# Kernel optimization log

Measured on AMD Instinct MI355X. Metric: run time of the kernel, lower is better.

## Reference

```python
import jax, jax.numpy as jnp
import numpy as np

STRIDES = (2, 2, 2)  # from init strides
BN_EPS = 1e-3        # keras BatchNormalization default epsilon


def upsample3d(x, s):
    # x: [B, D, H, W, C] -> nearest-neighbor repeat, like keras UpSampling3D
    x = jnp.repeat(x, s[0], axis=1)
    x = jnp.repeat(x, s[1], axis=2)
    return jnp.repeat(x, s[2], axis=3)


def _conv3d_same(xi, wi):
    # xi: [D, H, W, C]; wi: [kd, kh, kw, Cin, Cout] -> SAME, stride 1
    return jax.lax.conv_general_dilated(
        xi[None], wi, window_strides=(1, 1, 1), padding='SAME',
        dimension_numbers=('NDHWC', 'DHWIO', 'NDHWC'))[0]


# per-sample dynamic conv: each batch element uses its own hypernet kernel
per_sample_conv3d = jax.vmap(_conv3d_same, in_axes=(0, 0))


def batchnorm_train(x, gamma, beta):
    # training-mode BN over N,D,H,W axes
    mean = jnp.mean(x, axis=(0, 1, 2, 3), keepdims=True)
    var = jnp.var(x, axis=(0, 1, 2, 3), keepdims=True)
    return gamma * (x - mean) * jax.lax.rsqrt(var + BN_EPS) + beta


def setup_inputs() -> dict:
    key = jax.random.key(0)
    k1, k2, k3, k4 = jax.random.split(key, 4)
    B, D, H, W, Cin, Cmid = 4, 8, 32, 32, 128, 64
    x = jax.random.normal(k1, (B, D, H, W, Cin), dtype=jnp.float32)
    # scale kernels like fan-in init to keep activations sane
    w1 = jax.random.normal(k2, (B, 3, 3, 3, Cin, Cmid), dtype=jnp.float32) * 0.02
    w2 = jax.random.normal(k3, (B, 3, 3, 3, 2 * Cmid, Cmid), dtype=jnp.float32) * 0.02
    skip = jax.random.normal(k4, (B, 2 * D, 2 * H, 2 * W, Cmid), dtype=jnp.float32)
    return {
        'x': x, 'w1': w1, 'w2': w2, 'skip': skip,
        'gamma1': jnp.ones((Cmid,), jnp.float32),
        'beta1': jnp.zeros((Cmid,), jnp.float32),
        'gamma2': jnp.ones((Cmid,), jnp.float32),
        'beta2': jnp.zeros((Cmid,), jnp.float32),
        'training': 1,
    }


def reference(x, w1, w2, skip, gamma1, beta1, gamma2, beta2, training):
    x = upsample3d(x, STRIDES)                       # [B, 2D, 2H, 2W, Cin]
    x = per_sample_conv3d(x, w1)                     # [B, 2D, 2H, 2W, Cmid]
    x = batchnorm_train(x, gamma1, beta1)
    x = jax.nn.relu(x)
    x = jnp.concatenate([x, skip], axis=-1)          # [B, 2D, 2H, 2W, 2*Cmid]
    x = per_sample_conv3d(x, w2)                     # [B, 2D, 2H, 2W, Cmid]
    x = batchnorm_train(x, gamma2, beta2)
    return jax.nn.relu(x)
```

## Files before the change

kernel.cpp:

```cpp
#include <hip/hip_runtime.h>


typedef __attribute__((ext_vector_type(8))) short short8;
typedef __attribute__((ext_vector_type(4))) float f32x4;

__device__ __forceinline__ float bf2f(unsigned short u) {
  union { unsigned int i; float f; } v; v.i = ((unsigned int)u) << 16; return v.f;
}
__device__ __forceinline__ unsigned short f2b(float f) {
  union { float ff; unsigned int u; } v; v.ff = f;
  unsigned int x = v.u;
  return (unsigned short)((x + 0x7FFFu + ((x >> 16) & 1u)) >> 16);
}
__device__ __forceinline__ unsigned int pk2(float a, float b) {
  return (unsigned int)f2b(a) | ((unsigned int)f2b(b) << 16);
}
__device__ __forceinline__ void gload16(const void* g, void* l) {
  __builtin_amdgcn_global_load_lds(
      (const __attribute__((address_space(1))) void*)g,
      (__attribute__((address_space(3))) void*)l, 16, 0, 0);
}

#define ASTR 136
#define WSTR 132

__global__ __launch_bounds__(256) void hg_prep_k(
    const float* __restrict__ x, const float* __restrict__ skip,
    const float* __restrict__ w1, const float* __restrict__ w2,
    unsigned short* __restrict__ xb, unsigned short* __restrict__ skb,
    unsigned short* __restrict__ wt2, unsigned short* __restrict__ wc1,
    float* __restrict__ sums) {
  __shared__ short T[64 * ASTR];
  int blk = blockIdx.x;
  int tid = threadIdx.x;
  if (blk < 10240) {
    const float* s; unsigned short* d; size_t i;
    if (blk < 8192) { s = skip; d = skb; i = ((size_t)blk * 256 + tid) << 3; }
    else            { s = x;    d = xb;  i = ((size_t)(blk - 8192) * 256 + tid) << 3; }
    float4 a = *(const float4*)(s + i);
    float4 c = *(const float4*)(s + i + 4);
    uint4 o;
    o.x = pk2(a.x, a.y); o.y = pk2(a.z, a.w);
    o.z = pk2(c.x, c.y); o.w = pk2(c.z, c.w);
    *(uint4*)(d + i) = o;
  } else if (blk < 10348) {
    int bt = blk - 10240;
    const float* src = w2 + (size_t)bt * 8192;
    int co = tid & 63, c0 = tid >> 6;
    for (int i = 0; i < 32; ++i) {
      int ci = c0 + (i << 2);
      T[co * ASTR + ci] = (short)f2b(src[(size_t)ci * 64 + co]);
    }
    __syncthreads();
    unsigned short* dst = wt2 + (size_t)bt * 8192;
    for (int i = 0; i < 4; ++i) {
      int task = tid + (i << 8);
      int row = task >> 4, q = task & 15;
      *(uint4*)(dst + row * 128 + (q << 3)) = *(const uint4*)&T[row * ASTR + (q << 3)];
    }
  } else if (blk < 10604) {
    int m9 = blk - 10348;
    int b = m9 >> 6, m = m9 & 63;
    int dd = m >> 4, hh = (m >> 2) & 3, ww = m & 3;
    const int ks[4] = {0, 1, 0, 2}, kc[4] = {1, 2, 2, 1};
    int co = tid & 63, c0 = tid >> 6;
    const float* wb = w1 + (size_t)b * 27 * 8192;
    for (int i = 0; i < 32; ++i) {
      int ci = c0 + (i << 2);
      float s = 0.f;
      for (int a = 0; a < kc[dd]; ++a)
        for (int e = 0; e < kc[hh]; ++e)
          for (int c = 0; c < kc[ww]; ++c) {
            int tap = ((ks[dd] + a) * 3 + ks[hh] + e) * 3 + ks[ww] + c;
            s += wb[(size_t)tap * 8192 + (size_t)ci * 64 + co];
          }
      T[co * ASTR + ci] = (short)f2b(s);
    }
    __syncthreads();
    unsigned short* dst = wc1 + (size_t)m9 * 8192;
    for (int i = 0; i < 4; ++i) {
      int task = tid + (i << 8);
      int row = task >> 4, q = task & 15;
      *(uint4*)(dst + row * 128 + (q << 3)) = *(const uint4*)&T[row * ASTR + (q << 3)];
    }
  } else {
    for (int i = tid; i < 2112; i += 256) sums[i] = 0.f;
  }
}

__global__ __launch_bounds__(256, 3) void hg_c1p_k(
    const unsigned short* __restrict__ xb, const unsigned short* __restrict__ wc1,
    const unsigned short* __restrict__ zb, unsigned short* __restrict__ outb,
    float* __restrict__ sums) {
  __shared__ short Xl[2 * 100 * 128];
  int tid = threadIdx.x;
  int xcd = blockIdx.x & 7, slot = blockIdx.x >> 3;
  int b = xcd & 3;
  int t = ((xcd >> 2) << 7) + slot;
  int od = t >> 4, hti = (t >> 2) & 3, wti = t & 3;
  int pd = od & 1, md = od >> 1;
  int lane = tid & 63, quad = lane >> 4, l16 = lane & 15;
  int wid = tid >> 6;
  int ph = wid >> 1, pw = wid & 1;

  for (int pl = 0; pl < 2; ++pl) {
    int sd = md + pd - 1 + pl;
    int dok = ((unsigned)sd < 8u);
    for (int i = 0; i < 7; ++i) {
      int task = tid + (i << 8);
      if (task < 1600) {
        int pos = task >> 4, pq = task & 15;
        int q = (pq & 8) | ((pq & 7) ^ (pos & 7));
        int sh = pos / 10, sw = pos - sh * 10;
        int h = (hti << 3) + sh - 1, w = (wti << 3) + sw - 1;
        const unsigned short* src = zb;
        if (dok && (unsigned)h < 32u && (unsigned)w < 32u)
          src = xb + ((((size_t)(b * 8 + sd)) * 32 + h) * 32 + w) * 128 + (q << 3);
        gload16(src, (char*)Xl + ((pl * 1600 + (i << 8) + (tid & 192)) << 4));
      }
    }
  }
  __syncthreads();

  f32x4 acc[4][4];
#pragma unroll
  for (int i = 0; i < 4; ++i)
#pragma unroll
    for (int j = 0; j < 4; ++j) acc[i][j] = (f32x4){0.f, 0.f, 0.f, 0.f};

  const unsigned short* wcb = wc1 + ((size_t)b * 64 + (pd << 5) + (ph << 3) + (pw << 1)) * 8192;

  for (int td = 0; td < 2; ++td) {
    const char* Xp = (const char*)Xl + td * 25600;
    for (int th = 0; th < 2; ++th) {
      int hb = ph + th;
      for (int tw = 0; tw < 2; ++tw) {
        int wb2 = pw + tw;
        const unsigned short* wp = wcb + (size_t)((td << 4) + (th << 2) + tw) * 8192;
#pragma unroll
        for (int ksx = 0; ksx < 4; ++ksx) {
          int cq = (ksx << 2) + quad;
          short8 av[4], bv[4];
#pragma unroll
          for (int mt = 0; mt < 4; ++mt) {
            int pos = ((mt << 1) + (l16 >> 3) + hb) * 10 + (l16 & 7) + wb2;
            int pc = (cq & 8) | ((cq & 7) ^ (pos & 7));
            av[mt] = *(const short8*)(Xp + pos * 256 + (pc << 4));
          }
#pragma unroll
          for (int nt = 0; nt < 4; ++nt)
            bv[nt] = *(const short8*)(wp + ((nt << 4) + l16) * 128 + (cq << 3));
#pragma unroll
          for (int mt = 0; mt < 4; ++mt)
#pragma unroll
            for (int nt = 0; nt < 4; ++nt)
              acc[mt][nt] = __builtin_amdgcn_mfma_f32_16x16x32_bf16(
                  av[mt], bv[nt], acc[mt][nt], 0, 0, 0);
        }
      }
    }
  }

  __syncthreads();
  float* sbf = (float*)Xl;
  int rowb = (b * 16 + od) * 64;
#pragma unroll
  for (int nt = 0; nt < 4; ++nt) {
    int n = (nt << 4) + l16;
    float s = 0.f, q2 = 0.f;
#pragma unroll
    for (int mt = 0; mt < 4; ++mt) {
      int mh = (mt << 1) + (quad >> 1);
      int oh = (((hti << 3) + mh) << 1) + ph;
      size_t rb = (size_t)(rowb + oh) * 64;
#pragma unroll
      for (int r = 0; r < 4; ++r) {
        float v = acc[mt][nt][r];
        int ow = (((wti << 3) + ((quad & 1) << 2) + r) << 1) + pw;
        outb[(rb + ow) * 64 + n] = f2b(v);
        s += v; q2 += v * v;
      }
    }
    s += __shfl_xor(s, 16); s += __shfl_xor(s, 32);
    q2 += __shfl_xor(q2, 16); q2 += __shfl_xor(q2, 32);
    if (quad == 0) { sbf[wid * 128 + n] = s; sbf[wid * 128 + 64 + n] = q2; }
  }
  __syncthreads();
  if (tid < 64) {
    float s = sbf[tid] + sbf[128 + tid] + sbf[256 + tid] + sbf[384 + tid];
    float q2 = sbf[64 + tid] + sbf[192 + tid] + sbf[320 + tid] + sbf[448 + tid];
    int sl = (blockIdx.x & 7) << 7;
    atomicAdd(&sums[sl + tid], s);
    atomicAdd(&sums[sl + 64 + tid], q2);
  }
}

__global__ __launch_bounds__(256) void hg_convf_k(
    const unsigned short* __restrict__ y1n, const unsigned short* __restrict__ skb,
    const unsigned short* __restrict__ wt, const unsigned short* __restrict__ zb,
    float* __restrict__ outf, float* __restrict__ sums) {
  __shared__ short Al[132 * 128];
  __shared__ short Wl[64 * 128];
  int tid = threadIdx.x;
  int xcd = blockIdx.x & 7, slot = blockIdx.x >> 3;
  int b = xcd & 3;
  int t = ((xcd >> 2) << 8) + slot;
  int m0 = (b << 16) + (t << 7);
  int od  = (t >> 5) & 15;
  int oh0 = (t << 1) & 63;
  int lane = tid & 63, quad = lane >> 4, l16 = lane & 15;
  int wm = (tid >> 6) << 5;

  f32x4 acc[2][4];
  for (int i = 0; i < 2; ++i)
    for (int j = 0; j < 4; ++j) acc[i][j] = (f32x4){0.f, 0.f, 0.f, 0.f};

  const unsigned short* wb = wt + (size_t)b * 27 * 8192;

  for (int kd = 0; kd < 3; ++kd) {
    int ud = od + kd - 1;
    int dok = ((unsigned)ud < 16u);
    for (int kh = 0; kh < 3; ++kh) {
      __syncthreads();
      for (int i = 0; i < 9; ++i) {
        int task = tid + (i << 8);
        if (task < 2112) {
          int pos = task >> 4, pq = task & 15;
          int q = (pq & 8) | ((pq & 7) ^ (pos & 7));
          int g = (pos >= 66) ? 1 : 0;
          int uw = pos - (g ? 66 : 0) - 1;
          int uh = oh0 + g + kh - 1;
          const unsigned short* src = zb;
          if (dok && (unsigned)uh < 64u && (unsigned)uw < 64u) {
            size_t srow = (((size_t)(b * 16 + ud)) * 64 + uh) * 64 + uw;
            src = (q < 8) ? (y1n + srow * 64 + (q << 3))
                          : (skb + srow * 64 + ((q - 8) << 3));
          }
          gload16(src, (char*)Al + (((i << 8) + (tid & 192)) << 4));
        }
      }
      for (int kw = 0; kw < 3; ++kw) {
        if (kw) __syncthreads();
        int tap = (kd * 3 + kh) * 3 + kw;
        const unsigned short* wsrc = wb + (size_t)tap * 8192;
        {
          int co0 = tid >> 4, pq = tid & 15;
          for (int i = 0; i < 4; ++i) {
            int co = co0 + (i << 4);
            int q = (pq & 8) | ((pq & 7) ^ (co & 7));
            gload16(wsrc + co * 128 + (q << 3),
                    (char*)Wl + (((i << 8) + (tid & 192)) << 4));
          }
        }
        __syncthreads();
        for (int k0 = 0; k0 < 128; k0 += 32) {
          int cq = (k0 >> 3) + quad;
          short8 av[2], bv[4];
          for (int mt = 0; mt < 2; ++mt) {
            int r = wm + (mt << 4) + l16;
            int pos = (r >> 6) * 66 + (r & 63) + kw;
            int pc = (cq & 8) | ((cq & 7) ^ (pos & 7));
            av[mt] = *(const short8*)((const char*)Al + pos * 256 + (pc << 4));
          }
          for (int nt = 0; nt < 4; ++nt) {
            int co = (nt << 4) + l16;
            int pc = (cq & 8) | ((cq & 7) ^ (co & 7));
            bv[nt] = *(const short8*)((const char*)Wl + co * 256 + (pc << 4));
          }
          for (int mt = 0; mt < 2; ++mt)
            for (int nt = 0; nt < 4; ++nt)
              acc[mt][nt] = __builtin_amdgcn_mfma_f32_16x16x32_bf16(
                  av[mt], bv[nt], acc[mt][nt], 0, 0, 0);
        }
      }
    }
  }

  __syncthreads();
  float* sbf = (float*)Al;
  for (int nt = 0; nt < 4; ++nt) {
    int n = (nt << 4) + l16;
    float s = 0.f, q2 = 0.f;
    for (int mt = 0; mt < 2; ++mt) {
      int mbase = m0 + wm + (mt << 4) + (quad << 2);
      for (int r = 0; r < 4; ++r) {
        float v = acc[mt][nt][r];
        outf[(size_t)(mbase + r) * 64 + n] = v;
        s += v; q2 += v * v;
      }
    }
    s += __shfl_xor(s, 16); s += __shfl_xor(s, 32);
    q2 += __shfl_xor(q2, 16); q2 += __shfl_xor(q2, 32);
    if (quad == 0) { sbf[(wm >> 5) * 128 + n] = s; sbf[(wm >> 5) * 128 + 64 + n] = q2; }
  }
  __syncthreads();
  if (tid < 64) {
    float s = sbf[tid] + sbf[128 + tid] + sbf[256 + tid] + sbf[384 + tid];
    float q2 = sbf[64 + tid] + sbf[192 + tid] + sbf[320 + tid] + sbf[448 + tid];
    int sl = (blockIdx.x & 7) << 7;
    atomicAdd(&sums[sl + tid], s);
    atomicAdd(&sums[sl + 64 + tid], q2);
  }
}

__global__ __launch_bounds__(256) void hg_bnbf_k(unsigned short* __restrict__ y,
                                                 const float* __restrict__ sb,
                                                 const float* __restrict__ gm,
                                                 const float* __restrict__ bt) {
  __shared__ float sc[64], sh[64];
  int tid = threadIdx.x;
  if (tid < 64) {
    float s = 0.f, q2 = 0.f;
    for (int k = 0; k < 8; ++k) { s += sb[(k << 7) + tid]; q2 += sb[(k << 7) + 64 + tid]; }
    float invN = 1.f / 262144.f;
    float mean = s * invN;
    float var  = q2 * invN - mean * mean;
    float scl = gm[tid] * rsqrtf(var + 1e-3f);
    sc[tid] = scl; sh[tid] = bt[tid] - mean * scl;
  }
  __syncthreads();
  size_t i = ((size_t)blockIdx.x * 256 + tid) << 3;
  int c0 = (int)(i & 63);
  uint4 v = *(uint4*)(y + i);
  unsigned int u[4] = {v.x, v.y, v.z, v.w};
  for (int q = 0; q < 4; ++q) {
    int c = c0 + q * 2;
    float f0 = sc[c] * bf2f((unsigned short)(u[q] & 0xFFFFu)) + sh[c];
    float f1 = sc[c + 1] * bf2f((unsigned short)(u[q] >> 16)) + sh[c + 1];
    u[q] = pk2(f0 > 0.f ? f0 : 0.f, f1 > 0.f ? f1 : 0.f);
  }
  *(uint4*)(y + i) = make_uint4(u[0], u[1], u[2], u[3]);
}

__global__ __launch_bounds__(256) void hg_bnrf_k(float* __restrict__ y,
                                                 const float* __restrict__ sb,
                                                 const float* __restrict__ gm,
                                                 const float* __restrict__ bt) {
  __shared__ float sc[64], sh[64];
  int tid = threadIdx.x;
  if (tid < 64) {
    float s = 0.f, q2 = 0.f;
    for (int k = 0; k < 8; ++k) { s += sb[(k << 7) + tid]; q2 += sb[(k << 7) + 64 + tid]; }
    float invN = 1.f / 262144.f;
    float mean = s * invN;
    float var  = q2 * invN - mean * mean;
    float scl = gm[tid] * rsqrtf(var + 1e-3f);
    sc[tid] = scl; sh[tid] = bt[tid] - mean * scl;
  }
  __syncthreads();
  size_t i = (size_t)blockIdx.x * 256 + tid;
  int c4 = ((int)i & 15) << 2;
  float4 v = *(float4*)(y + i * 4);
  float f;
  f = sc[c4]     * v.x + sh[c4];     v.x = f > 0.f ? f : 0.f;
  f = sc[c4 + 1] * v.y + sh[c4 + 1]; v.y = f > 0.f ? f : 0.f;
  f = sc[c4 + 2] * v.z + sh[c4 + 2]; v.z = f > 0.f ? f : 0.f;
  f = sc[c4 + 3] * v.w + sh[c4 + 3]; v.w = f > 0.f ? f : 0.f;
  *(float4*)(y + i * 4) = v;
}

__global__ __launch_bounds__(256) void hg_wt_k(const float* __restrict__ w1,
                                               const float* __restrict__ w2,
                                               unsigned short* __restrict__ wt1,
                                               unsigned short* __restrict__ wt2) {
  __shared__ short T[64 * ASTR];
  int blk = blockIdx.x;
  int sel = blk >= 108;
  const float* w = sel ? w2 : w1;
  unsigned short* wt = sel ? wt2 : wt1;
  int bt = sel ? blk - 108 : blk;
  const float* src = w + (size_t)bt * 8192;
  int tid = threadIdx.x;
  int co = tid & 63;
  int c0 = tid >> 6;
  for (int i = 0; i < 32; ++i) {
    int ci = c0 + (i << 2);
    T[co * ASTR + ci] = (short)f2b(src[(size_t)ci * 64 + co]);
  }
  __syncthreads();
  unsigned short* dst = wt + (size_t)bt * 8192;
  for (int i = 0; i < 4; ++i) {
    int task = tid + (i << 8);
    int row = task >> 4, q = task & 15;
    *(uint4*)(dst + row * 128 + (q << 3)) = *(const uint4*)&T[row * ASTR + (q << 3)];
  }
}

__global__ __launch_bounds__(256) void hg_conv_o_k(
    const float* __restrict__ xf, const unsigned short* __restrict__ y1n,
    const float* __restrict__ skip, const float* __restrict__ wf,
    const unsigned short* __restrict__ wt, const float* __restrict__ bn,
    unsigned short* __restrict__ outb, float* __restrict__ outf,
    int mode, int has_wt) {
  __shared__ short Al[132 * ASTR];
  __shared__ short Wl[64 * WSTR];
  __shared__ float sbl[128];
  int tid = threadIdx.x;
  int xcd = blockIdx.x & 7, slot = blockIdx.x >> 3;
  int b = xcd & 3;
  int t = ((xcd >> 2) << 8) + slot;
  int m0 = (b << 16) + (t << 7);
  int od  = (t >> 5) & 15;
  int oh0 = (t << 1) & 63;
  int lane = tid & 63, quad = lane >> 4, l16 = lane & 15;
  int wm = (tid >> 6) << 5;

  if (mode == 1 && tid < 128) sbl[tid] = bn[tid];

  f32x4 acc[2][4];
  for (int i = 0; i < 2; ++i)
    for (int j = 0; j < 4; ++j) acc[i][j] = (f32x4){0.f, 0.f, 0.f, 0.f};

  const float* wbf = wf + (size_t)b * 27 * 8192;
  const unsigned short* wbt = wt + (size_t)b * 27 * 8192;

  for (int kd = 0; kd < 3; ++kd) {
    int ud = od + kd - 1;
    int dok = (ud >= 0 && ud < 16);
    for (int kh = 0; kh < 3; ++kh) {
      __syncthreads();
      for (int i = 0; i < 9; ++i) {
        int task = tid + (i << 8);
        if (task < 2112) {
          int chunk = task & 15;
          int pos = task >> 4;
          int g = (pos >= 66) ? 1 : 0;
          int uwi = pos - (g ? 66 : 0);
          int uh = oh0 + g + kh - 1;
          int uw = uwi - 1;
          uint4 val = make_uint4(0u, 0u, 0u, 0u);
          if (dok && (unsigned)uh < 64u && (unsigned)uw < 64u) {
            if (mode == 0) {
              size_t src = ((((size_t)(b * 8 + (ud >> 1))) * 32 + (uh >> 1)) * 32 +
                            (uw >> 1)) * 128 + (chunk << 3);
              float4 f0 = *(const float4*)(xf + src);
              float4 f1 = *(const float4*)(xf + src + 4);
              val.x = pk2(f0.x, f0.y); val.y = pk2(f0.z, f0.w);
              val.z = pk2(f1.x, f1.y); val.w = pk2(f1.z, f1.w);
            } else {
              size_t srow = (((size_t)(b * 16 + ud)) * 64 + uh) * 64 + uw;
              if (chunk < 8) {
                uint4 raw = *(const uint4*)(y1n + srow * 64 + (chunk << 3));
                unsigned int u[4] = {raw.x, raw.y, raw.z, raw.w};
                unsigned int o[4];
                int c0 = chunk << 3;
                for (int q = 0; q < 4; ++q) {
                  int c = c0 + q * 2;
                  float f0 = sbl[c] * bf2f((unsigned short)(u[q] & 0xFFFFu)) + sbl[64 + c];
                  float f1 = sbl[c + 1] * bf2f((unsigned short)(u[q] >> 16)) + sbl[64 + c + 1];
                  o[q] = pk2(f0 > 0.f ? f0 : 0.f, f1 > 0.f ? f1 : 0.f);
                }
                val = make_uint4(o[0], o[1], o[2], o[3]);
              } else {
                const float* sp = skip + srow * 64 + ((chunk - 8) << 3);
                float4 f0 = *(const float4*)(sp);
                float4 f1 = *(const float4*)(sp + 4);
                val.x = pk2(f0.x, f0.y); val.y = pk2(f0.z, f0.w);
                val.z = pk2(f1.x, f1.y); val.w = pk2(f1.z, f1.w);
              }
            }
          }
          *(uint4*)&Al[pos * ASTR + (chunk << 3)] = val;
        }
      }
      for (int kw = 0; kw < 3; ++kw) {
        if (kw) __syncthreads();
        int tap = (kd * 3 + kh) * 3 + kw;
        if (has_wt) {
          const unsigned short* wsrc = wbt + (size_t)tap * 8192;
          for (int i = 0; i < 4; ++i) {
            int task = tid + (i << 8);
            int co = task >> 4, q = task & 15;
            *(uint4*)&Wl[co * WSTR + (q << 3)] = *(const uint4*)(wsrc + co * 128 + (q << 3));
          }
        } else {
          const float* wp = wbf + (size_t)tap * 8192 + (tid & 63);
          int wco = tid & 63;
          int ci0 = (tid >> 6) << 5;
          for (int c = 0; c < 32; c += 2) {
            float f0 = wp[(size_t)(ci0 + c) * 64];
            float f1 = wp[(size_t)(ci0 + c + 1) * 64];
            *(unsigned int*)&Wl[wco * WSTR + ci0 + c] = pk2(f0, f1);
          }
        }
        __syncthreads();
        for (int k0 = 0; k0 < 128; k0 += 32) {
          int kk = k0 + (quad << 3);
          union { uint4 u; short8 s; } cv;
          short8 av[2];
          for (int mt = 0; mt < 2; ++mt) {
            int r = wm + (mt << 4) + l16;
            int g = r >> 6, ow = r & 63;
            cv.u = *(const uint4*)&Al[(g * 66 + ow + kw) * ASTR + kk];
            av[mt] = cv.s;
          }
          short8 bv[4];
          for (int nt = 0; nt < 4; ++nt) {
            int base = ((nt << 4) + l16) * WSTR + kk;
            uint2 lo = *(const uint2*)&Wl[base];
            uint2 hi = *(const uint2*)&Wl[base + 4];
            cv.u = make_uint4(lo.x, lo.y, hi.x, hi.y);
            bv[nt] = cv.s;
          }
          for (int mt = 0; mt < 2; ++mt)
            for (int nt = 0; nt < 4; ++nt)
              acc[mt][nt] = __builtin_amdgcn_mfma_f32_16x16x32_bf16(
                  av[mt], bv[nt], acc[mt][nt], 0, 0, 0);
        }
      }
    }
  }

  for (int mt = 0; mt < 2; ++mt) {
    int mbase = m0 + wm + (mt << 4) + (quad << 2);
    for (int nt = 0; nt < 4; ++nt) {
      int n = (nt << 4) + l16;
      for (int r = 0; r < 4; ++r) {
        float v = acc[mt][nt][r];
        size_t o = (size_t)(mbase + r) * 64 + n;
        if (mode == 0) outb[o] = f2b(v);
        else outf[o] = v;
      }
    }
  }
}

__global__ void hg_zero_k(float* __restrict__ p, int n) {
  for (int i = threadIdx.x; i < n; i += 256) p[i] = 0.f;
}

__global__ __launch_bounds__(256) void hg_stats_k(const unsigned short* __restrict__ yb,
                                                  const float* __restrict__ yf, int isf,
                                                  float* __restrict__ sums) {
  int t = threadIdx.x;
  int c = t & 63;
  int r0 = blockIdx.x * 4 + (t >> 6);
  float sum = 0.f, ss = 0.f;
  for (int r = r0; r < 262144; r += 4096) {
    size_t idx = (size_t)r * 64 + c;
    float v = isf ? yf[idx] : bf2f(yb[idx]);
    sum += v; ss += v * v;
  }
  atomicAdd(&sums[c], sum);
  atomicAdd(&sums[64 + c], ss);
}

__global__ void hg_fin_k(float* __restrict__ sb, const float* __restrict__ gm,
                         const float* __restrict__ bt) {
  int c = threadIdx.x;
  float invN = 1.f / 262144.f;
  float mean = sb[c] * invN;
  float var  = sb[64 + c] * invN - mean * mean;
  float sc = gm[c] * rsqrtf(var + 1e-3f);
  sb[c] = sc;
  sb[64 + c] = bt[c] - mean * sc;
}

__global__ __launch_bounds__(256) void hg_bnb_k(unsigned short* __restrict__ y,
                                                const float* __restrict__ sb) {
  size_t i = ((size_t)blockIdx.x * 256 + threadIdx.x) << 3;
  int c0 = (int)(i & 63);
  uint4 v = *(uint4*)(y + i);
  unsigned int u[4] = {v.x, v.y, v.z, v.w};
  for (int q = 0; q < 4; ++q) {
    int c = c0 + q * 2;
    float f0 = sb[c] * bf2f((unsigned short)(u[q] & 0xFFFFu)) + sb[64 + c];
    float f1 = sb[c + 1] * bf2f((unsigned short)(u[q] >> 16)) + sb[64 + c + 1];
    u[q] = pk2(f0 > 0.f ? f0 : 0.f, f1 > 0.f ? f1 : 0.f);
  }
  *(uint4*)(y + i) = make_uint4(u[0], u[1], u[2], u[3]);
}

__global__ __launch_bounds__(256) void hg_bnrelu_f_k(float* __restrict__ y,
                                                     const float* __restrict__ sb) {
  size_t i = (size_t)blockIdx.x * 256 + threadIdx.x;
  int c4 = ((int)i & 15) << 2;
  float4 v = *(float4*)(y + i * 4);
  float f;
  f = sb[c4]     * v.x + sb[64 + c4];     v.x = f > 0.f ? f : 0.f;
  f = sb[c4 + 1] * v.y + sb[64 + c4 + 1]; v.y = f > 0.f ? f : 0.f;
  f = sb[c4 + 2] * v.z + sb[64 + c4 + 2]; v.z = f > 0.f ? f : 0.f;
  f = sb[c4 + 3] * v.w + sb[64 + c4 + 3]; v.w = f > 0.f ? f : 0.f;
  *(float4*)(y + i * 4) = v;
}

extern "C" void kernel_launch(void* const* d_in, const int* in_sizes, int n_in,
                              void* d_out, int out_size, void* d_ws, size_t ws_size,
                              hipStream_t stream) {
  (void)out_size;
  int ix = 0, iw1 = 1, iw2 = 2, isk = 3, ig1 = 4, ib1 = 5, ig2 = 6, ib2 = 7;
  if (n_in >= 9 && in_sizes[0] == 4194304 && in_sizes[1] == 884736 &&
      in_sizes[3] == 16777216 && in_sizes[4] == 64) {
  } else if (n_in >= 9 && in_sizes[0] == 64 && in_sizes[4] == 16777216 &&
             in_sizes[6] == 884736 && in_sizes[8] == 4194304) {
    ib1 = 0; ib2 = 1; ig1 = 2; ig2 = 3; isk = 4; iw1 = 6; iw2 = 7; ix = 8;
  } else {
    return;
  }
  if (ws_size < (32ull << 20) + 2048ull) return;

  const float* x    = (const float*)d_in[ix];
  const float* w1   = (const float*)d_in[iw1];
  const float* w2   = (const float*)d_in[iw2];
  const float* skip = (const float*)d_in[isk];
  const float* g1   = (const float*)d_in[ig1];
  const float* b1   = (const float*)d_in[ib1];
  const float* g2   = (const float*)d_in[ig2];
  const float* b2   = (const float*)d_in[ib2];
  float* out = (float*)d_out;

  const size_t OFF_SUMS = 32ull << 20;
  const size_t OFF_ZB   = OFF_SUMS + 8192;
  const size_t OFF_WT2  = OFF_ZB + 256;
  const size_t OFF_XB   = OFF_WT2 + 2ull * 1769472;
  const size_t OFF_SKB  = OFF_XB + 8388608;
  const size_t OFF_WC1  = OFF_SKB + 33554432;
  const size_t NEED     = OFF_WC1 + 4194304;

  unsigned short* y1 = (unsigned short*)d_ws;

  if (ws_size >= NEED) {
    float* sums  = (float*)((char*)d_ws + OFF_SUMS);
    float* sums1 = sums;
    float* sums2 = sums + 1024;
    unsigned short* zb  = (unsigned short*)((char*)d_ws + OFF_ZB);
    unsigned short* wt2 = (unsigned short*)((char*)d_ws + OFF_WT2);
    unsigned short* xb  = (unsigned short*)((char*)d_ws + OFF_XB);
    unsigned short* skb = (unsigned short*)((char*)d_ws + OFF_SKB);
    unsigned short* wc1 = (unsigned short*)((char*)d_ws + OFF_WC1);

    hg_prep_k<<<10605, 256, 0, stream>>>(x, skip, w1, w2, xb, skb, wt2, wc1, sums);
    hg_c1p_k<<<1024, 256, 0, stream>>>(xb, wc1, zb, y1, sums1);
    hg_bnbf_k<<<8192, 256, 0, stream>>>(y1, sums1, g1, b1);
    hg_convf_k<<<2048, 256, 0, stream>>>(y1, skb, wt2, zb, out, sums2);
    hg_bnrf_k<<<16384, 256, 0, stream>>>(out, sums2, g2, b2);
  } else {
    float* sums  = (float*)((char*)d_ws + (32ull << 20));
    float* sums1 = sums;
    float* sums2 = sums + 128;
    unsigned short* wt1 = (unsigned short*)((char*)d_ws + (32ull << 20) + 2048ull);
    unsigned short* wt2 = wt1 + 884736ull;
    const size_t WS_NEED = (32ull << 20) + 2048ull + 2ull * 884736ull * 2ull;
    int has_wt = (ws_size >= WS_NEED) ? 1 : 0;

    hg_zero_k<<<1, 256, 0, stream>>>(sums, 512);
    if (has_wt) hg_wt_k<<<216, 256, 0, stream>>>(w1, w2, wt1, wt2);
    hg_conv_o_k<<<2048, 256, 0, stream>>>(x, y1, skip, w1, wt1, sums1, y1, out, 0, has_wt);
    hg_stats_k<<<1024, 256, 0, stream>>>(y1, out, 0, sums1);
    hg_fin_k<<<1, 64, 0, stream>>>(sums1, g1, b1);
    hg_conv_o_k<<<2048, 256, 0, stream>>>(x, y1, skip, w2, wt2, sums1, y1, out, 1, has_wt);
    hg_stats_k<<<1024, 256, 0, stream>>>(y1, out, 1, sums2);
    hg_fin_k<<<1, 64, 0, stream>>>(sums2, g2, b2);
    hg_bnrelu_f_k<<<16384, 256, 0, stream>>>(out, sums2);
  }
}
```

Before: 423.5 us.

## Switch second conv to 32x32x16 MFMA with split-K across waves

Moves the second conv kernel from 16x16x32 to 32x32x16 bf16 MFMA tiles. The four waves are rearranged into two M halves times two K halves, and the partial sums are reduced through shared memory before the store and the BN statistics. The larger tiles need fewer LDS fragment reads per FLOP, which cuts LDS traffic per MFMA. The cost is an extra LDS reduction pass and barrier, and only half the waves do the epilogue.

```diff
diff --git a/kernel.cpp b/kernel.cpp
--- a/kernel.cpp
+++ b/kernel.cpp
@@ -3,6 +3,7 @@
 
 typedef __attribute__((ext_vector_type(8))) short short8;
 typedef __attribute__((ext_vector_type(4))) float f32x4;
+typedef __attribute__((ext_vector_type(16))) float f32x16;
 
 __device__ __forceinline__ float bf2f(unsigned short u) {
   union { unsigned int i; float f; } v; v.i = ((unsigned int)u) << 16; return v.f;
@@ -208,12 +209,16 @@
   int m0 = (b << 16) + (t << 7);
   int od  = (t >> 5) & 15;
   int oh0 = (t << 1) & 63;
-  int lane = tid & 63, quad = lane >> 4, l16 = lane & 15;
-  int wm = (tid >> 6) << 5;
-
-  f32x4 acc[2][4];
-  for (int i = 0; i < 2; ++i)
-    for (int j = 0; j < 4; ++j) acc[i][j] = (f32x4){0.f, 0.f, 0.f, 0.f};
+  int lane = tid & 63, l32 = lane & 31, lh = lane >> 5;
+  int wid = tid >> 6;
+  int wh = wid & 1;
+  int ks = wid >> 1;
+
+  f32x16 acc[2][2];
+#pragma unroll
+  for (int e = 0; e < 16; ++e) {
+    acc[0][0][e] = 0.f; acc[0][1][e] = 0.f; acc[1][0][e] = 0.f; acc[1][1][e] = 0.f;
+  }
 
   const unsigned short* wb = wt + (size_t)b * 27 * 8192;
 
@@ -253,23 +258,28 @@
           }
         }
         __syncthreads();
-        for (int k0 = 0; k0 < 128; k0 += 32) {
-          int cq = (k0 >> 3) + quad;
-          short8 av[2], bv[4];
+#pragma unroll
+        for (int kt = 0; kt < 4; ++kt) {
+          int ch = (ks << 3) + (kt << 1) + lh;
+          short8 av[2], bv[2];
+#pragma unroll
           for (int mt = 0; mt < 2; ++mt) {
-            int r = wm + (mt << 4) + l16;
+            int r = (wh << 6) + (mt << 5) + l32;
             int pos = (r >> 6) * 66 + (r & 63) + kw;
-            int pc = (cq & 8) | ((cq & 7) ^ (pos & 7));
+            int pc = (ch & 8) | ((ch & 7) ^ (pos & 7));
             av[mt] = *(const short8*)((const char*)Al + pos * 256 + (pc << 4));
           }
-          for (int nt = 0; nt < 4; ++nt) {
-            int co = (nt << 4) + l16;
-            int pc = (cq & 8) | ((cq & 7) ^ (co & 7));
+#pragma unroll
+          for (int nt = 0; nt < 2; ++nt) {
+            int co = (nt << 5) + l32;
+            int pc = (ch & 8) | ((ch & 7) ^ (co & 7));
             bv[nt] = *(const short8*)((const char*)Wl + co * 256 + (pc << 4));
           }
+#pragma unroll
           for (int mt = 0; mt < 2; ++mt)
-            for (int nt = 0; nt < 4; ++nt)
-              acc[mt][nt] = __builtin_amdgcn_mfma_f32_16x16x32_bf16(
+#pragma unroll
+            for (int nt = 0; nt < 2; ++nt)
+              acc[mt][nt] = __builtin_amdgcn_mfma_f32_32x32x16_bf16(
                   av[mt], bv[nt], acc[mt][nt], 0, 0, 0);
         }
       }
@@ -277,26 +287,57 @@
   }
 
   __syncthreads();
-  float* sbf = (float*)Al;
-  for (int nt = 0; nt < 4; ++nt) {
-    int n = (nt << 4) + l16;
-    float s = 0.f, q2 = 0.f;
-    for (int mt = 0; mt < 2; ++mt) {
-      int mbase = m0 + wm + (mt << 4) + (quad << 2);
-      for (int r = 0; r < 4; ++r) {
-        float v = acc[mt][nt][r];
-        outf[(size_t)(mbase + r) * 64 + n] = v;
-        s += v; q2 += v * v;
-      }
-    }
-    s += __shfl_xor(s, 16); s += __shfl_xor(s, 32);
-    q2 += __shfl_xor(q2, 16); q2 += __shfl_xor(q2, 32);
-    if (quad == 0) { sbf[(wm >> 5) * 128 + n] = s; sbf[(wm >> 5) * 128 + 64 + n] = q2; }
+  if (ks == 1) {
+    char* base = (char*)Al + (((wh << 6) + lane) << 4);
+#pragma unroll
+    for (int mt = 0; mt < 2; ++mt)
+#pragma unroll
+      for (int nt = 0; nt < 2; ++nt)
+#pragma unroll
+        for (int r4 = 0; r4 < 4; ++r4) {
+          f32x4 v = {acc[mt][nt][(r4 << 2)], acc[mt][nt][(r4 << 2) + 1],
+                     acc[mt][nt][(r4 << 2) + 2], acc[mt][nt][(r4 << 2) + 3]};
+          *(f32x4*)(base + ((((mt << 1) + nt) << 2) + r4) * 2048) = v;
+        }
+  }
+  __syncthreads();
+  float* sbf = (float*)Wl;
+  if (ks == 0) {
+    const char* base = (const char*)Al + (((wh << 6) + lane) << 4);
+#pragma unroll
+    for (int mt = 0; mt < 2; ++mt)
+#pragma unroll
+      for (int nt = 0; nt < 2; ++nt)
+#pragma unroll
+        for (int r4 = 0; r4 < 4; ++r4) {
+          f32x4 v = *(const f32x4*)(base + ((((mt << 1) + nt) << 2) + r4) * 2048);
+#pragma unroll
+          for (int j = 0; j < 4; ++j) acc[mt][nt][(r4 << 2) + j] += v[j];
+        }
+#pragma unroll
+    for (int nt = 0; nt < 2; ++nt) {
+      int n = (nt << 5) + l32;
+      float s = 0.f, q2 = 0.f;
+#pragma unroll
+      for (int mt = 0; mt < 2; ++mt) {
+        int rbase = m0 + (wh << 6) + (mt << 5) + (lh << 2);
+#pragma unroll
+        for (int r = 0; r < 16; ++r) {
+          float v = acc[mt][nt][r];
+          int row = rbase + (r & 3) + ((r >> 2) << 3);
+          outf[(size_t)row * 64 + n] = v;
+          s += v; q2 += v * v;
+        }
+      }
+      s += __shfl_xor(s, 32);
+      q2 += __shfl_xor(q2, 32);
+      if (lh == 0) { sbf[(wh << 7) + n] = s; sbf[(wh << 7) + 64 + n] = q2; }
+    }
   }
   __syncthreads();
   if (tid < 64) {
-    float s = sbf[tid] + sbf[128 + tid] + sbf[256 + tid] + sbf[384 + tid];
-    float q2 = sbf[64 + tid] + sbf[192 + tid] + sbf[320 + tid] + sbf[448 + tid];
+    float s = sbf[tid] + sbf[128 + tid];
+    float q2 = sbf[64 + tid] + sbf[192 + tid];
     int sl = (blockIdx.x & 7) << 7;
     atomicAdd(&sums[sl + tid], s);
     atomicAdd(&sums[sl + 64 + tid], q2);
```

Result: no change. 422.8 us (-0.2%).
